# Performance work log

Hardware: AMD Instinct MI355X
Metric: run time of the kernel (lower is better)

## Reference

```python
import jax, jax.numpy as jnp
import numpy as np

N_NODES = 100000
N_EDGES = 1600000
IN_D = 128
OUT_D = 128


def setup_inputs() -> dict:
    key = jax.random.key(0)
    ks = jax.random.split(key, 10)
    scale = 1.0 / np.sqrt(IN_D)
    inp = {
        "x": jax.random.normal(ks[0], (N_NODES, IN_D), dtype=jnp.float32),
        "edge_idx": jax.random.randint(ks[1], (2, N_EDGES), 0, N_NODES, dtype=jnp.int32),
        "W1": jax.random.normal(ks[2], (OUT_D, IN_D), dtype=jnp.float32) * scale,
        "b1": jax.random.normal(ks[3], (OUT_D,), dtype=jnp.float32) * scale,
        "W2": jax.random.normal(ks[4], (OUT_D, IN_D), dtype=jnp.float32) * scale,
        "b2": jax.random.normal(ks[5], (OUT_D,), dtype=jnp.float32) * scale,
        "W3": jax.random.normal(ks[6], (OUT_D, IN_D), dtype=jnp.float32) * scale,
        "b3": jax.random.normal(ks[7], (OUT_D,), dtype=jnp.float32) * scale,
        "W4": jax.random.normal(ks[8], (OUT_D, IN_D), dtype=jnp.float32) * scale,
        "b4": jax.random.normal(ks[9], (OUT_D,), dtype=jnp.float32) * scale,
    }
    return inp


def _message_passing(y, src, dst, num_nodes, add_self=True):
    # original: if add_self: x = x + x  (doubles features)
    if add_self:
        y = y + y
    # gather messages from source nodes, scatter-add into target nodes
    return jax.ops.segment_sum(y[src], dst, num_segments=num_nodes)


def reference(x, edge_idx, W1, b1, W2, b2, W3, b3, W4, b4):
    num_nodes = x.shape[0]
    src, dst = edge_idx[0], edge_idx[1]
    x1 = x @ W1.T + b1
    x2 = _message_passing(x @ W2.T + b2, src, dst, num_nodes)
    x3 = _message_passing(x @ W3.T + b3, src, dst, num_nodes)
    x4 = _message_passing(x @ W4.T + b4, src, dst, num_nodes)
    return jax.nn.sigmoid(x3 + x4) * x2 + x1
```

## Files before the change

kernel.cpp:

```cpp
#include <hip/hip_runtime.h>

__device__ __forceinline__ float bf2f(unsigned short u) {
    union { unsigned int i; float f; } v;
    v.i = ((unsigned int)u) << 16;
    return v.f;
}
__device__ __forceinline__ unsigned short f2bf(float f) {
    union { float f; unsigned int i; } v;
    v.f = f;
    unsigned int x = v.i;
    return (unsigned short)((x + 0x7fffu + ((x >> 16) & 1u)) >> 16);
}

typedef short bf16x8 __attribute__((ext_vector_type(8)));
typedef float f32x4 __attribute__((ext_vector_type(4)));

#define BSHIFT 9
#define BRANGE 512

__global__ __launch_bounds__(256) void prep_hist_kernel(
    const float* __restrict__ x,
    const float* __restrict__ W1, const float* __restrict__ W2,
    const float* __restrict__ W3, const float* __restrict__ W4,
    unsigned short* __restrict__ xb, unsigned short* __restrict__ Wb,
    const int* __restrict__ dst, int* __restrict__ bpart,
    int M, int nx4, int ne)
{
    __shared__ int h[256];
    const int t = threadIdx.x;
    const int blk = blockIdx.x;
    const bool histBlock = (blk < 256);
    if (histBlock) {
        h[t] = 0;
        __syncthreads();
    }

    int i = blk * 256 + t;
    if (i < nx4) {
        float4 v = ((const float4*)x)[i];
        unsigned lo = (unsigned)f2bf(v.x) | ((unsigned)f2bf(v.y) << 16);
        unsigned hi = (unsigned)f2bf(v.z) | ((unsigned)f2bf(v.w) << 16);
        uint2 p; p.x = lo; p.y = hi;
        *(uint2*)(xb + (size_t)i * 4) = p;
    }
    if (i < 16384) {
        Wb[i]         = f2bf(W1[i]);
        Wb[16384 + i] = f2bf(W2[i]);
        Wb[32768 + i] = f2bf(W3[i] + W4[i]);
    }

    if (histBlock) {
        for (int e = blk * 256 + t; e < ne; e += 65536)
            atomicAdd(&h[dst[e] >> BSHIFT], 1);
        __syncthreads();
        bpart[blk * 256 + t] = h[t];
    }
}

__global__ __launch_bounds__(256) void bucket_scan_kernel(
    const int* __restrict__ bpart, int* __restrict__ boff, int* __restrict__ gcur, int nb)
{
    __shared__ int sh[256];
    int t = threadIdx.x;
    int v = 0;
    for (int k = 0; k < 256; ++k) v += bpart[k * 256 + t];
    if (t >= nb) v = 0;
    sh[t] = v;
    __syncthreads();
    int acc = v;
    for (int off = 1; off < 256; off <<= 1) {
        int y = (t >= off) ? sh[t - off] : 0;
        __syncthreads();
        acc += y;
        sh[t] = acc;
        __syncthreads();
    }
    if (t < nb) {
        boff[t + 1] = acc;
        gcur[t] = acc - v;
    }
    if (t == 0) boff[0] = 0;
}

__global__ __launch_bounds__(512) void bucketize_kernel(
    const int* __restrict__ src, const int* __restrict__ dst,
    int* __restrict__ gcur, int2* __restrict__ bucketed, int ne, int chunk)
{
    __shared__ int cnt[256];
    __shared__ int sbase[256];
    const int t = threadIdx.x;
    const int e0 = blockIdx.x * chunk;
    const int e1 = (e0 + chunk < ne) ? e0 + chunk : ne;

    if (t < 256) cnt[t] = 0;
    __syncthreads();
    for (int e = e0 + t; e < e1; e += 512)
        atomicAdd(&cnt[dst[e] >> BSHIFT], 1);
    __syncthreads();
    if (t < 256) {
        int c = cnt[t];
        sbase[t] = c ? atomicAdd(&gcur[t], c) : 0;
        cnt[t] = 0;
    }
    __syncthreads();
    for (int e = e0 + t; e < e1; e += 512) {
        int d = dst[e];
        int b = d >> BSHIFT;
        int loc = atomicAdd(&cnt[b], 1);
        int2 v; v.x = src[e]; v.y = d;
        bucketed[sbase[b] + loc] = v;
    }
}

__global__ __launch_bounds__(512) void bucket_finalize_kernel(
    const int2* __restrict__ bucketed, const int* __restrict__ boff,
    int* __restrict__ offs, int* __restrict__ deg, int* __restrict__ csr,
    int M, int nb)
{
    __shared__ int cnt[BRANGE];
    __shared__ int sc[BRANGE];
    const int t = threadIdx.x;
    const int b = blockIdx.x;
    cnt[t] = 0;
    __syncthreads();
    const int lo = boff[b], hi = boff[b + 1];
    for (int i = lo + t; i < hi; i += 512)
        atomicAdd(&cnt[bucketed[i].y & (BRANGE - 1)], 1);
    __syncthreads();
    const int v = cnt[t];
    sc[t] = v;
    __syncthreads();
    int acc = v;
    for (int off = 1; off < 512; off <<= 1) {
        int y = (t >= off) ? sc[t - off] : 0;
        __syncthreads();
        acc += y;
        sc[t] = acc;
        __syncthreads();
    }
    const int excl = acc - v;
    const int node = (b << BSHIFT) + t;
    if (node < M) {
        offs[node] = lo + excl;
        deg[node] = v;
    }
    if (b == nb - 1 && t == 0) offs[M] = hi;
    cnt[t] = lo + excl;
    __syncthreads();
    for (int i = lo + t; i < hi; i += 512) {
        int2 e = bucketed[i];
        int p = atomicAdd(&cnt[e.y & (BRANGE - 1)], 1);
        csr[p] = e.x;
    }
}

__global__ void prep_kernel(const float* __restrict__ x,
                            const float* __restrict__ W1, const float* __restrict__ W2,
                            const float* __restrict__ W3, const float* __restrict__ W4,
                            unsigned short* __restrict__ xb, unsigned short* __restrict__ Wb,
                            int* __restrict__ deg, int M, int nx4)
{
    int i = blockIdx.x * 256 + threadIdx.x;
    if (i < nx4) {
        float4 v = ((const float4*)x)[i];
        unsigned lo = (unsigned)f2bf(v.x) | ((unsigned)f2bf(v.y) << 16);
        unsigned hi = (unsigned)f2bf(v.z) | ((unsigned)f2bf(v.w) << 16);
        uint2 p; p.x = lo; p.y = hi;
        *(uint2*)(xb + (size_t)i * 4) = p;
    }
    if (deg && i < M) deg[i] = 0;
    if (i < 16384) {
        Wb[i]         = f2bf(W1[i]);
        Wb[16384 + i] = f2bf(W2[i]);
        Wb[32768 + i] = f2bf(W3[i] + W4[i]);
    }
}

__global__ void hist_kernel(const int* __restrict__ dst, int* __restrict__ deg, int ne) {
    int e = blockIdx.x * blockDim.x + threadIdx.x;
    if (e < ne) atomicAdd(&deg[dst[e]], 1);
}

__global__ __launch_bounds__(1024) void scan_local_kernel(
    const int* __restrict__ deg, int* __restrict__ offs, int* __restrict__ bsum, int n)
{
    __shared__ int sh[1024];
    int t = threadIdx.x;
    int i = blockIdx.x * 1024 + t;
    int v = (i < n) ? deg[i] : 0;
    sh[t] = v;
    __syncthreads();
    int acc = v;
    for (int off = 1; off < 1024; off <<= 1) {
        int y = (t >= off) ? sh[t - off] : 0;
        __syncthreads();
        acc += y;
        sh[t] = acc;
        __syncthreads();
    }
    if (i < n) offs[i] = acc - v;
    if (t == 1023) bsum[blockIdx.x] = acc;
}

__global__ __launch_bounds__(128) void scan_totals_kernel(
    int* __restrict__ bsum, int* __restrict__ offs, int nb, int n)
{
    __shared__ int sh[128];
    int t = threadIdx.x;
    int v = (t < nb) ? bsum[t] : 0;
    sh[t] = v;
    __syncthreads();
    int acc = v;
    for (int off = 1; off < 128; off <<= 1) {
        int y = (t >= off) ? sh[t - off] : 0;
        __syncthreads();
        acc += y;
        sh[t] = acc;
        __syncthreads();
    }
    if (t < nb) bsum[t] = acc - v;
    if (t == 127) offs[n] = acc;
}

__global__ __launch_bounds__(1024) void scan_finalize_kernel(
    int* __restrict__ offs, const int* __restrict__ bsum, int* __restrict__ cursor, int n)
{
    int i = blockIdx.x * 1024 + threadIdx.x;
    if (i < n) {
        int o = offs[i] + bsum[i >> 10];
        offs[i] = o;
        if (cursor) cursor[i] = o;
    }
}

__global__ __launch_bounds__(256) void fill_csr_ranged_kernel(
    const int* __restrict__ src, const int* __restrict__ dst,
    int* __restrict__ cursor, int* __restrict__ csr, int ne, int rangeSize)
{
    const int r = blockIdx.x & 7;
    const int cb = blockIdx.x >> 3;
    const int nchunk = gridDim.x >> 3;
    const unsigned lo = (unsigned)(r * rangeSize);
    for (int e = cb * 256 + threadIdx.x; e < ne; e += nchunk * 256) {
        int d = dst[e];
        int s = src[e];
        if ((unsigned)(d - lo) < (unsigned)rangeSize) {
            int pos = atomicAdd(&cursor[d], 1);
            csr[pos] = s;
        }
    }
}

template<bool BF16SRC>
__global__ __launch_bounds__(256) void gather_kernel(
    const void* __restrict__ xsrc, const int* __restrict__ offs,
    const int* __restrict__ csr, unsigned short* __restrict__ gb, int M)
{
    const int wave = threadIdx.x >> 6;
    const int lane = threadIdx.x & 63;
    const int node = blockIdx.x * 4 + wave;
    if (node >= M) return;
    const int e0 = offs[node];
    const int e1 = offs[node + 1];

    float s0 = 0.f, s1 = 0.f, t0 = 0.f, t1 = 0.f;
    for (int e = e0; e < e1; e += 8) {
        int id[8];
        float m[8];
#pragma unroll
        for (int j = 0; j < 8; ++j) {
            int ee = e + j;
            bool ok = ee < e1;
            id[j] = csr[ok ? ee : e1 - 1];
            m[j] = ok ? 1.f : 0.f;
        }
#pragma unroll
        for (int j = 0; j < 8; ++j) {
            float lo, hi;
            if (BF16SRC) {
                unsigned v = *(const unsigned*)((const unsigned short*)xsrc +
                                                (size_t)id[j] * 128 + lane * 2);
                lo = bf2f((unsigned short)(v & 0xffffu));
                hi = bf2f((unsigned short)(v >> 16));
            } else {
                float2 v = *(const float2*)((const float*)xsrc +
                                            (size_t)id[j] * 128 + lane * 2);
                lo = v.x;
                hi = v.y;
            }
            if (j & 1) { t0 += m[j] * lo; t1 += m[j] * hi; }
            else       { s0 += m[j] * lo; s1 += m[j] * hi; }
        }
    }
    unsigned pk = (unsigned)f2bf(s0 + t0) | ((unsigned)f2bf(s1 + t1) << 16);
    *(unsigned*)(gb + (size_t)node * 128 + lane * 2) = pk;
}

template<bool XBF16>
__global__ __launch_bounds__(256) void gemm_kernel(
    const void* __restrict__ xsrc, const unsigned short* __restrict__ gb,
    const int* __restrict__ deg, const unsigned short* __restrict__ Wb,
    const float* __restrict__ B1, const float* __restrict__ B2,
    const float* __restrict__ B3, const float* __restrict__ B4,
    float* __restrict__ out, int M)
{
    __shared__ unsigned short x_lds[32 * 136];
    __shared__ unsigned short g_lds[32 * 136];

    const int t = threadIdx.x;
    const int wave = t >> 6;
    const int lane = t & 63;
    const int ln = lane & 15;
    const int quad = lane >> 4;
    const int row0 = blockIdx.x * 32;

    if (XBF16) {
        const unsigned short* xb = (const unsigned short*)xsrc;
#pragma unroll
        for (int i = 0; i < 2; ++i) {
            int c = i * 256 + t;
            int row = c >> 4;
            int koff = (c & 15) * 8;
            int grow = row0 + row;
            if (grow > M - 1) grow = M - 1;
            *(uint4*)&x_lds[row * 136 + koff] =
                *(const uint4*)(xb + (size_t)grow * 128 + koff);
        }
    } else {
        const float* xf = (const float*)xsrc;
#pragma unroll
        for (int i = 0; i < 4; ++i) {
            int c = i * 256 + t;
            int row = c >> 5;
            int koff = (c & 31) * 4;
            int grow = row0 + row;
            if (grow > M - 1) grow = M - 1;
            float4 v = *(const float4*)(xf + (size_t)grow * 128 + koff);
            unsigned p0 = (unsigned)f2bf(v.x) | ((unsigned)f2bf(v.y) << 16);
            unsigned p1 = (unsigned)f2bf(v.z) | ((unsigned)f2bf(v.w) << 16);
            *(unsigned*)&x_lds[row * 136 + koff]     = p0;
            *(unsigned*)&x_lds[row * 136 + koff + 2] = p1;
        }
    }
#pragma unroll
    for (int i = 0; i < 2; ++i) {
        int c = i * 256 + t;
        int row = c >> 4;
        int koff = (c & 15) * 8;
        int grow = row0 + row;
        if (grow > M - 1) grow = M - 1;
        *(uint4*)&g_lds[row * 136 + koff] =
            *(const uint4*)(gb + (size_t)grow * 128 + koff);
    }
    __syncthreads();

    f32x4 acc[3][2][2];
#pragma unroll
    for (int p = 0; p < 3; ++p)
#pragma unroll
        for (int rt = 0; rt < 2; ++rt)
#pragma unroll
            for (int c = 0; c < 2; ++c) {
                acc[p][rt][c][0] = 0.f; acc[p][rt][c][1] = 0.f;
                acc[p][rt][c][2] = 0.f; acc[p][rt][c][3] = 0.f;
            }

#pragma unroll
    for (int kk = 0; kk < 4; ++kk) {
        bf16x8 ax[2], ag[2];
#pragma unroll
        for (int rt = 0; rt < 2; ++rt) {
            ax[rt] = *(const bf16x8*)&x_lds[(rt * 16 + ln) * 136 + kk * 32 + quad * 8];
            ag[rt] = *(const bf16x8*)&g_lds[(rt * 16 + ln) * 136 + kk * 32 + quad * 8];
        }
#pragma unroll
        for (int p = 0; p < 3; ++p) {
#pragma unroll
            for (int c = 0; c < 2; ++c) {
                int col = wave * 32 + c * 16 + ln;
                bf16x8 bw = *(const bf16x8*)(Wb + (size_t)p * 16384 +
                                             (size_t)col * 128 + kk * 32 + quad * 8);
#pragma unroll
                for (int rt = 0; rt < 2; ++rt) {
                    acc[p][rt][c] = __builtin_amdgcn_mfma_f32_16x16x32_bf16(
                        (p == 0) ? ax[rt] : ag[rt], bw, acc[p][rt][c], 0, 0, 0);
                }
            }
        }
    }

#pragma unroll
    for (int rt = 0; rt < 2; ++rt) {
#pragma unroll
        for (int i = 0; i < 4; ++i) {
            int row = row0 + rt * 16 + quad * 4 + i;
            if (row < M) {
                float dg = (float)deg[row];
#pragma unroll
                for (int c = 0; c < 2; ++c) {
                    int col = wave * 32 + c * 16 + ln;
                    float p1 = acc[0][rt][c][i] + B1[col];
                    float h2 = 2.f * (acc[1][rt][c][i] + dg * B2[col]);
                    float z  = 2.f * (acc[2][rt][c][i] + dg * (B3[col] + B4[col]));
                    float g = 1.f / (1.f + __expf(-z));
                    out[(size_t)row * 128 + col] = g * h2 + p1;
                }
            }
        }
    }
}

extern "C" void kernel_launch(void* const* d_in, const int* in_sizes, int n_in,
                              void* d_out, int out_size, void* d_ws, size_t ws_size,
                              hipStream_t stream) {
    const float* x  = (const float*)d_in[0];
    const int* eidx = (const int*)d_in[1];
    const float* W1 = (const float*)d_in[2];
    const float* B1 = (const float*)d_in[3];
    const float* W2 = (const float*)d_in[4];
    const float* B2 = (const float*)d_in[5];
    const float* W3 = (const float*)d_in[6];
    const float* B3 = (const float*)d_in[7];
    const float* W4 = (const float*)d_in[8];
    const float* B4 = (const float*)d_in[9];
    float* out      = (float*)d_out;

    const int M  = in_sizes[0] / 128;
    const int NE = in_sizes[1] / 2;
    const int* src = eidx;
    const int* dst = eidx + NE;

    const int NB = (M + BRANGE - 1) >> BSHIFT;

    auto pad = [](size_t b) { return (b + 127) & ~(size_t)127; };
    const size_t xb_bytes  = pad((size_t)M * 128 * 2);
    const size_t gb_bytes  = pad((size_t)M * 128 * 2);
    const size_t wb_bytes  = pad((size_t)3 * 16384 * 2);
    const size_t deg_bytes = pad((size_t)M * 4);
    const size_t off_bytes = pad((size_t)(M + 1) * 4);
    const size_t csr_bytes = pad((size_t)NE * 4);
    const size_t bkt_bytes = pad((size_t)NE * 8);
    const size_t bpart_bytes = pad((size_t)256 * 256 * 4);

    const size_t need_full = xb_bytes + gb_bytes + wb_bytes + deg_bytes + off_bytes +
                             csr_bytes + bkt_bytes + bpart_bytes + 4 * 1024;
    const bool full = (NB <= 256) && ws_size >= need_full + 1024;

    char* ws = (char*)d_ws;
    size_t off = 0;
    auto take = [&](size_t bytes) -> char* {
        char* p = ws + off;
        off = (off + bytes + 127) & ~(size_t)127;
        return p;
    };

    const int nbScan = (M + 1023) / 1024;

    if (full) {
        unsigned short* xb = (unsigned short*)take(xb_bytes);
        unsigned short* gb = (unsigned short*)take(gb_bytes);
        unsigned short* Wb = (unsigned short*)take(wb_bytes);
        int* deg    = (int*)take((size_t)M * 4);
        int* offs   = (int*)take((size_t)(M + 1) * 4);
        int* csr    = (int*)take((size_t)NE * 4);
        int2* bkt   = (int2*)take((size_t)NE * 8);
        int* bpart  = (int*)take((size_t)256 * 256 * 4);
        int* boff   = (int*)take(257 * 4);
        int* gcur   = (int*)take(256 * 4);

        const int nx4 = M * 128 / 4;
        const int chunk = (NE + 255) / 256;
        int prep_grid = (M * 32 + 255) / 256;
        if (prep_grid < 256) prep_grid = 256;

        prep_hist_kernel<<<prep_grid, 256, 0, stream>>>(
            x, W1, W2, W3, W4, xb, Wb, dst, bpart, M, nx4, NE);
        bucket_scan_kernel<<<1, 256, 0, stream>>>(bpart, boff, gcur, NB);
        bucketize_kernel<<<256, 512, 0, stream>>>(src, dst, gcur, bkt, NE, chunk);
        bucket_finalize_kernel<<<NB, 512, 0, stream>>>(bkt, boff, offs, deg, csr, M, NB);
        gather_kernel<true><<<(M + 3) / 4, 256, 0, stream>>>(xb, offs, csr, gb, M);
        gemm_kernel<true><<<(M + 31) / 32, 256, 0, stream>>>(
            xb, gb, deg, Wb, B1, B2, B3, B4, out, M);
    } else {
        unsigned short* gb = (unsigned short*)take(gb_bytes);
        unsigned short* Wb = (unsigned short*)take(wb_bytes);
        int* deg    = (int*)take((size_t)M * 4);
        int* offs   = (int*)take((size_t)(M + 1) * 4);
        int* cursor = (int*)take((size_t)M * 4);
        int* bsum   = (int*)take(256 * 4);
        int* csr    = (int*)take((size_t)NE * 4);

        const int prep_elems = (M > 16384 ? M : 16384);
        const int rangeSize = (M + 7) / 8;
        prep_kernel<<<(prep_elems + 255) / 256, 256, 0, stream>>>(
            x, W1, W2, W3, W4, nullptr, Wb, deg, M, 0);
        hist_kernel<<<(NE + 255) / 256, 256, 0, stream>>>(dst, deg, NE);
        scan_local_kernel<<<nbScan, 1024, 0, stream>>>(deg, offs, bsum, M);
        scan_totals_kernel<<<1, 128, 0, stream>>>(bsum, offs, nbScan, M);
        scan_finalize_kernel<<<nbScan, 1024, 0, stream>>>(offs, bsum, cursor, M);
        fill_csr_ranged_kernel<<<2048, 256, 0, stream>>>(src, dst, cursor, csr, NE, rangeSize);
        gather_kernel<false><<<(M + 3) / 4, 256, 0, stream>>>(x, offs, csr, gb, M);
        gemm_kernel<false><<<(M + 31) / 32, 256, 0, stream>>>(
            x, gb, deg, Wb, B1, B2, B3, B4, out, M);
    }
}
```

Baseline: 282.1 us.

## Make GEMM persistent with double-buffered LDS prefetch and pre-permuted weights

```diff
diff --git a/kernel.cpp b/kernel.cpp
--- a/kernel.cpp
+++ b/kernel.cpp
@@ -17,6 +17,13 @@
 
 #define BSHIFT 9
 #define BRANGE 512
+
+__device__ __forceinline__ int wperm(int i) {
+    int col = i >> 7, k = i & 127;
+    int cg = col >> 4, lnw = col & 15;
+    int kkw = k >> 5, qw = (k >> 3) & 3, ew = k & 7;
+    return (((cg * 4 + kkw) * 64) + qw * 16 + lnw) * 8 + ew;
+}
 
 __global__ __launch_bounds__(256) void prep_hist_kernel(
     const float* __restrict__ x,
@@ -44,9 +51,10 @@
         *(uint2*)(xb + (size_t)i * 4) = p;
     }
     if (i < 16384) {
-        Wb[i]         = f2bf(W1[i]);
-        Wb[16384 + i] = f2bf(W2[i]);
-        Wb[32768 + i] = f2bf(W3[i] + W4[i]);
+        int off = wperm(i);
+        Wb[off]         = f2bf(W1[i]);
+        Wb[16384 + off] = f2bf(W2[i]);
+        Wb[32768 + off] = f2bf(W3[i] + W4[i]);
     }
 
     if (histBlock) {
@@ -170,9 +178,10 @@
     }
     if (deg && i < M) deg[i] = 0;
     if (i < 16384) {
-        Wb[i]         = f2bf(W1[i]);
-        Wb[16384 + i] = f2bf(W2[i]);
-        Wb[32768 + i] = f2bf(W3[i] + W4[i]);
+        int off = wperm(i);
+        Wb[off]         = f2bf(W1[i]);
+        Wb[16384 + off] = f2bf(W2[i]);
+        Wb[32768 + off] = f2bf(W3[i] + W4[i]);
     }
 }
 
@@ -302,111 +311,156 @@
     const int* __restrict__ deg, const unsigned short* __restrict__ Wb,
     const float* __restrict__ B1, const float* __restrict__ B2,
     const float* __restrict__ B3, const float* __restrict__ B4,
-    float* __restrict__ out, int M)
-{
-    __shared__ unsigned short x_lds[32 * 136];
-    __shared__ unsigned short g_lds[32 * 136];
+    float* __restrict__ out, int M, int nTiles)
+{
+    __shared__ unsigned short x_lds[2][32 * 136];
+    __shared__ unsigned short g_lds[2][32 * 136];
 
     const int t = threadIdx.x;
     const int wave = t >> 6;
     const int lane = t & 63;
     const int ln = lane & 15;
     const int quad = lane >> 4;
-    const int row0 = blockIdx.x * 32;
-
-    if (XBF16) {
-        const unsigned short* xb = (const unsigned short*)xsrc;
-#pragma unroll
-        for (int i = 0; i < 2; ++i) {
-            int c = i * 256 + t;
-            int row = c >> 4;
-            int koff = (c & 15) * 8;
-            int grow = row0 + row;
-            if (grow > M - 1) grow = M - 1;
-            *(uint4*)&x_lds[row * 136 + koff] =
-                *(const uint4*)(xb + (size_t)grow * 128 + koff);
-        }
-    } else {
-        const float* xf = (const float*)xsrc;
-#pragma unroll
-        for (int i = 0; i < 4; ++i) {
-            int c = i * 256 + t;
-            int row = c >> 5;
-            int koff = (c & 31) * 4;
-            int grow = row0 + row;
-            if (grow > M - 1) grow = M - 1;
-            float4 v = *(const float4*)(xf + (size_t)grow * 128 + koff);
-            unsigned p0 = (unsigned)f2bf(v.x) | ((unsigned)f2bf(v.y) << 16);
-            unsigned p1 = (unsigned)f2bf(v.z) | ((unsigned)f2bf(v.w) << 16);
-            *(unsigned*)&x_lds[row * 136 + koff]     = p0;
-            *(unsigned*)&x_lds[row * 136 + koff + 2] = p1;
-        }
-    }
-#pragma unroll
-    for (int i = 0; i < 2; ++i) {
-        int c = i * 256 + t;
-        int row = c >> 4;
-        int koff = (c & 15) * 8;
-        int grow = row0 + row;
-        if (grow > M - 1) grow = M - 1;
-        *(uint4*)&g_lds[row * 136 + koff] =
-            *(const uint4*)(gb + (size_t)grow * 128 + koff);
-    }
-    __syncthreads();
-
-    f32x4 acc[3][2][2];
-#pragma unroll
-    for (int p = 0; p < 3; ++p)
-#pragma unroll
-        for (int rt = 0; rt < 2; ++rt)
-#pragma unroll
-            for (int c = 0; c < 2; ++c) {
-                acc[p][rt][c][0] = 0.f; acc[p][rt][c][1] = 0.f;
-                acc[p][rt][c][2] = 0.f; acc[p][rt][c][3] = 0.f;
+
+    const int r0c = t >> 4,          k0c = (t & 15) * 8;
+    const int r1c = (256 + t) >> 4,  k1c = ((256 + t) & 15) * 8;
+
+    int tile = blockIdx.x;
+    if (tile >= nTiles) return;
+    const int stride = gridDim.x;
+
+    uint4 rx0, rx1, rg0, rg1;
+    float4 f0, f1, f2, f3;
+
+    {
+        const int row0 = tile * 32;
+        if (XBF16) {
+            const unsigned short* xb = (const unsigned short*)xsrc;
+            int gr0 = row0 + r0c; if (gr0 > M - 1) gr0 = M - 1;
+            int gr1 = row0 + r1c; if (gr1 > M - 1) gr1 = M - 1;
+            rx0 = *(const uint4*)(xb + (size_t)gr0 * 128 + k0c);
+            rx1 = *(const uint4*)(xb + (size_t)gr1 * 128 + k1c);
+        } else {
+            const float* xf = (const float*)xsrc;
+            { int c = t;       int row = c >> 5, ko = (c & 31) * 4; int gr = row0 + row; if (gr > M - 1) gr = M - 1; f0 = *(const float4*)(xf + (size_t)gr * 128 + ko); }
+            { int c = 256 + t; int row = c >> 5, ko = (c & 31) * 4; int gr = row0 + row; if (gr > M - 1) gr = M - 1; f1 = *(const float4*)(xf + (size_t)gr * 128 + ko); }
+            { int c = 512 + t; int row = c >> 5, ko = (c & 31) * 4; int gr = row0 + row; if (gr > M - 1) gr = M - 1; f2 = *(const float4*)(xf + (size_t)gr * 128 + ko); }
+            { int c = 768 + t; int row = c >> 5, ko = (c & 31) * 4; int gr = row0 + row; if (gr > M - 1) gr = M - 1; f3 = *(const float4*)(xf + (size_t)gr * 128 + ko); }
+        }
+        int gr0 = row0 + r0c; if (gr0 > M - 1) gr0 = M - 1;
+        int gr1 = row0 + r1c; if (gr1 > M - 1) gr1 = M - 1;
+        rg0 = *(const uint4*)(gb + (size_t)gr0 * 128 + k0c);
+        rg1 = *(const uint4*)(gb + (size_t)gr1 * 128 + k1c);
+    }
+
+    int cur = 0;
+    for (;;) {
+        if (XBF16) {
+            *(uint4*)&x_lds[cur][r0c * 136 + k0c] = rx0;
+            *(uint4*)&x_lds[cur][r1c * 136 + k1c] = rx1;
+        } else {
+            { int c = t;       int row = c >> 5, ko = (c & 31) * 4;
+              unsigned p0 = (unsigned)f2bf(f0.x) | ((unsigned)f2bf(f0.y) << 16);
+              unsigned p1 = (unsigned)f2bf(f0.z) | ((unsigned)f2bf(f0.w) << 16);
+              *(unsigned*)&x_lds[cur][row * 136 + ko] = p0; *(unsigned*)&x_lds[cur][row * 136 + ko + 2] = p1; }
+            { int c = 256 + t; int row = c >> 5, ko = (c & 31) * 4;
+              unsigned p0 = (unsigned)f2bf(f1.x) | ((unsigned)f2bf(f1.y) << 16);
+              unsigned p1 = (unsigned)f2bf(f1.z) | ((unsigned)f2bf(f1.w) << 16);
+              *(unsigned*)&x_lds[cur][row * 136 + ko] = p0; *(unsigned*)&x_lds[cur][row * 136 + ko + 2] = p1; }
+            { int c = 512 + t; int row = c >> 5, ko = (c & 31) * 4;
+              unsigned p0 = (unsigned)f2bf(f2.x) | ((unsigned)f2bf(f2.y) << 16);
+              unsigned p1 = (unsigned)f2bf(f2.z) | ((unsigned)f2bf(f2.w) << 16);
+              *(unsigned*)&x_lds[cur][row * 136 + ko] = p0; *(unsigned*)&x_lds[cur][row * 136 + ko + 2] = p1; }
+            { int c = 768 + t; int row = c >> 5, ko = (c & 31) * 4;
+              unsigned p0 = (unsigned)f2bf(f3.x) | ((unsigned)f2bf(f3.y) << 16);
+              unsigned p1 = (unsigned)f2bf(f3.z) | ((unsigned)f2bf(f3.w) << 16);
+              *(unsigned*)&x_lds[cur][row * 136 + ko] = p0; *(unsigned*)&x_lds[cur][row * 136 + ko + 2] = p1; }
+        }
+        *(uint4*)&g_lds[cur][r0c * 136 + k0c] = rg0;
+        *(uint4*)&g_lds[cur][r1c * 136 + k1c] = rg1;
+        __syncthreads();
+
+        const int row0 = tile * 32;
+        const int nxt = tile + stride;
+        if (nxt < nTiles) {
+            const int nrow0 = nxt * 32;
+            if (XBF16) {
+                const unsigned short* xb = (const unsigned short*)xsrc;
+                int gr0 = nrow0 + r0c; if (gr0 > M - 1) gr0 = M - 1;
+                int gr1 = nrow0 + r1c; if (gr1 > M - 1) gr1 = M - 1;
+                rx0 = *(const uint4*)(xb + (size_t)gr0 * 128 + k0c);
+                rx1 = *(const uint4*)(xb + (size_t)gr1 * 128 + k1c);
+            } else {
+                const float* xf = (const float*)xsrc;
+                { int c = t;       int row = c >> 5, ko = (c & 31) * 4; int gr = nrow0 + row; if (gr > M - 1) gr = M - 1; f0 = *(const float4*)(xf + (size_t)gr * 128 + ko); }
+                { int c = 256 + t; int row = c >> 5, ko = (c & 31) * 4; int gr = nrow0 + row; if (gr > M - 1) gr = M - 1; f1 = *(const float4*)(xf + (size_t)gr * 128 + ko); }
+                { int c = 512 + t; int row = c >> 5, ko = (c & 31) * 4; int gr = nrow0 + row; if (gr > M - 1) gr = M - 1; f2 = *(const float4*)(xf + (size_t)gr * 128 + ko); }
+                { int c = 768 + t; int row = c >> 5, ko = (c & 31) * 4; int gr = nrow0 + row; if (gr > M - 1) gr = M - 1; f3 = *(const float4*)(xf + (size_t)gr * 128 + ko); }
             }
-
-#pragma unroll
-    for (int kk = 0; kk < 4; ++kk) {
-        bf16x8 ax[2], ag[2];
-#pragma unroll
-        for (int rt = 0; rt < 2; ++rt) {
-            ax[rt] = *(const bf16x8*)&x_lds[(rt * 16 + ln) * 136 + kk * 32 + quad * 8];
-            ag[rt] = *(const bf16x8*)&g_lds[(rt * 16 + ln) * 136 + kk * 32 + quad * 8];
-        }
-#pragma unroll
-        for (int p = 0; p < 3; ++p) {
-#pragma unroll
-            for (int c = 0; c < 2; ++c) {
-                int col = wave * 32 + c * 16 + ln;
-                bf16x8 bw = *(const bf16x8*)(Wb + (size_t)p * 16384 +
-                                             (size_t)col * 128 + kk * 32 + quad * 8);
-#pragma unroll
-                for (int rt = 0; rt < 2; ++rt) {
-                    acc[p][rt][c] = __builtin_amdgcn_mfma_f32_16x16x32_bf16(
-                        (p == 0) ? ax[rt] : ag[rt], bw, acc[p][rt][c], 0, 0, 0);
+            int gr0 = nrow0 + r0c; if (gr0 > M - 1) gr0 = M - 1;
+            int gr1 = nrow0 + r1c; if (gr1 > M - 1) gr1 = M - 1;
+            rg0 = *(const uint4*)(gb + (size_t)gr0 * 128 + k0c);
+            rg1 = *(const uint4*)(gb + (size_t)gr1 * 128 + k1c);
+        }
+
+        f32x4 acc[3][2][2];
+#pragma unroll
+        for (int p = 0; p < 3; ++p)
+#pragma unroll
+            for (int rt = 0; rt < 2; ++rt)
+#pragma unroll
+                for (int c = 0; c < 2; ++c) {
+                    acc[p][rt][c][0] = 0.f; acc[p][rt][c][1] = 0.f;
+                    acc[p][rt][c][2] = 0.f; acc[p][rt][c][3] = 0.f;
+                }
+
+#pragma unroll
+        for (int kk = 0; kk < 4; ++kk) {
+            bf16x8 ax[2], ag[2];
+#pragma unroll
+            for (int rt = 0; rt < 2; ++rt) {
+                ax[rt] = *(const bf16x8*)&x_lds[cur][(rt * 16 + ln) * 136 + kk * 32 + quad * 8];
+                ag[rt] = *(const bf16x8*)&g_lds[cur][(rt * 16 + ln) * 136 + kk * 32 + quad * 8];
+            }
+#pragma unroll
+            for (int p = 0; p < 3; ++p) {
+#pragma unroll
+                for (int c = 0; c < 2; ++c) {
+                    bf16x8 bw = *(const bf16x8*)(Wb +
+                        ((size_t)((p * 8 + wave * 2 + c) * 4 + kk) << 9) + lane * 8);
+#pragma unroll
+                    for (int rt = 0; rt < 2; ++rt) {
+                        acc[p][rt][c] = __builtin_amdgcn_mfma_f32_16x16x32_bf16(
+                            (p == 0) ? ax[rt] : ag[rt], bw, acc[p][rt][c], 0, 0, 0);
+                    }
                 }
             }
         }
-    }
-
-#pragma unroll
-    for (int rt = 0; rt < 2; ++rt) {
-#pragma unroll
-        for (int i = 0; i < 4; ++i) {
-            int row = row0 + rt * 16 + quad * 4 + i;
-            if (row < M) {
-                float dg = (float)deg[row];
-#pragma unroll
-                for (int c = 0; c < 2; ++c) {
-                    int col = wave * 32 + c * 16 + ln;
-                    float p1 = acc[0][rt][c][i] + B1[col];
-                    float h2 = 2.f * (acc[1][rt][c][i] + dg * B2[col]);
-                    float z  = 2.f * (acc[2][rt][c][i] + dg * (B3[col] + B4[col]));
-                    float g = 1.f / (1.f + __expf(-z));
-                    out[(size_t)row * 128 + col] = g * h2 + p1;
+
+#pragma unroll
+        for (int rt = 0; rt < 2; ++rt) {
+#pragma unroll
+            for (int i = 0; i < 4; ++i) {
+                int row = row0 + rt * 16 + quad * 4 + i;
+                if (row < M) {
+                    float dg = (float)deg[row];
+#pragma unroll
+                    for (int c = 0; c < 2; ++c) {
+                        int col = wave * 32 + c * 16 + ln;
+                        float p1 = acc[0][rt][c][i] + B1[col];
+                        float h2 = 2.f * (acc[1][rt][c][i] + dg * B2[col]);
+                        float z  = 2.f * (acc[2][rt][c][i] + dg * (B3[col] + B4[col]));
+                        float g = 1.f / (1.f + __expf(-z));
+                        __builtin_nontemporal_store(g * h2 + p1,
+                                                    &out[(size_t)row * 128 + col]);
+                    }
                 }
             }
         }
+
+        if (nxt >= nTiles) break;
+        tile = nxt;
+        cur ^= 1;
     }
 }
 
@@ -455,6 +509,8 @@
     };
 
     const int nbScan = (M + 1023) / 1024;
+    const int nTiles = (M + 31) / 32;
+    const int gemmGrid = nTiles < 1024 ? nTiles : 1024;
 
     if (full) {
         unsigned short* xb = (unsigned short*)take(xb_bytes);
@@ -479,8 +535,8 @@
         bucketize_kernel<<<256, 512, 0, stream>>>(src, dst, gcur, bkt, NE, chunk);
         bucket_finalize_kernel<<<NB, 512, 0, stream>>>(bkt, boff, offs, deg, csr, M, NB);
         gather_kernel<true><<<(M + 3) / 4, 256, 0, stream>>>(xb, offs, csr, gb, M);
-        gemm_kernel<true><<<(M + 31) / 32, 256, 0, stream>>>(
-            xb, gb, deg, Wb, B1, B2, B3, B4, out, M);
+        gemm_kernel<true><<<gemmGrid, 256, 0, stream>>>(
+            xb, gb, deg, Wb, B1, B2, B3, B4, out, M, nTiles);
     } else {
         unsigned short* gb = (unsigned short*)take(gb_bytes);
         unsigned short* Wb = (unsigned short*)take(wb_bytes);
@@ -500,7 +556,7 @@
         scan_finalize_kernel<<<nbScan, 1024, 0, stream>>>(offs, bsum, cursor, M);
         fill_csr_ranged_kernel<<<2048, 256, 0, stream>>>(src, dst, cursor, csr, NE, rangeSize);
         gather_kernel<false><<<(M + 3) / 4, 256, 0, stream>>>(x, offs, csr, gb, M);
-        gemm_kernel<false><<<(M + 31) / 32, 256, 0, stream>>>(
-            x, gb, deg, Wb, B1, B2, B3, B4, out, M);
-    }
-}
+        gemm_kernel<false><<<gemmGrid, 256, 0, stream>>>(
+            x, gb, deg, Wb, B1, B2, B3, B4, out, M, nTiles);
+    }
+}
```

Result: faster. 262.3 us (-7.0%).
